# Kernel optimization log

Hardware: AMD Instinct MI355X
Metric: run time of the kernel (lower is better)

The kernel has to match this reference:

```python
import jax, jax.numpy as jnp
import numpy as np
import math

D_MODEL = 512
N_HEADS = 8
WINDOW = 5
B, S = 4, 2048


def setup_inputs() -> dict:
    key = jax.random.key(0)
    ks = jax.random.split(key, 16)
    d = D_MODEL

    def lin(k, fan_in, fan_out):
        bound = 1.0 / math.sqrt(fan_in)
        kw, kb = jax.random.split(k)
        W = jax.random.uniform(kw, (fan_in, fan_out), jnp.float32, -bound, bound)
        b = jax.random.uniform(kb, (fan_out,), jnp.float32, -bound, bound)
        return W, b

    x = jax.random.normal(ks[0], (B, S, d), jnp.float32)
    W1, b1 = lin(ks[1], d, 2 * d)      # mapping layer 1
    W2, b2 = lin(ks[2], 2 * d, d)      # mapping layer 2
    Wq, bq = lin(ks[3], d, d)
    Wk, bk = lin(ks[4], d, d)
    Wv, bv = lin(ks[5], d, d)
    Wo, bo = lin(ks[6], d, d)
    return dict(x=x, W1=W1, b1=b1, W2=W2, b2=b2, Wq=Wq, bq=bq,
                Wk=Wk, bk=bk, Wv=Wv, bv=bv, Wo=Wo, bo=bo)


def reference(x, W1, b1, W2, b2, Wq, bq, Wk, bk, Wv, bv, Wo, bo):
    Bsz, S_, d = x.shape
    h = N_HEADS
    hd = d // h

    # mapping MLP: Linear -> ReLU -> Linear
    xm = jax.nn.relu(x @ W1 + b1) @ W2 + b2

    def split_heads(t):  # [B,S,d] -> [B,h,S,hd]
        return t.reshape(Bsz, S_, h, hd).transpose(0, 2, 1, 3)

    Q = split_heads(xm @ Wq + bq)
    K = split_heads(xm @ Wk + bk)
    V = split_heads(xm @ Wv + bv)

    scores = jnp.einsum('bhqd,bhkd->bhqk', Q, K) / math.sqrt(hd)

    # inverse sliding-window mask: positions with |i-j| <= window are EXCLUDED
    idx = jnp.arange(S_)
    adjacent = jnp.abs(idx[:, None] - idx[None, :]) <= WINDOW  # [S,S] bool
    scores = jnp.where(adjacent[None, None], -1e9, scores)

    attn = jax.nn.softmax(scores, axis=-1)
    out = jnp.einsum('bhqk,bhkd->bhqd', attn, V)
    out = out.transpose(0, 2, 1, 3).reshape(Bsz, S_, d)
    return out @ Wo + bo
```

## Files before the change

### kernel.cpp

```cpp
#include <hip/hip_runtime.h>
#include <stdint.h>

typedef __attribute__((ext_vector_type(8))) short bf16x8;
typedef __attribute__((ext_vector_type(4))) float f32x4;

__device__ __forceinline__ float bf2f(uint16_t u) {
    union { uint32_t u; float f; } c; c.u = ((uint32_t)u) << 16; return c.f;
}
__device__ __forceinline__ uint16_t f2bf(float f) {
    union { float f; uint32_t u; } c; c.f = f;
    uint32_t r = c.u + 0x7fffu + ((c.u >> 16) & 1u);
    return (uint16_t)(r >> 16);
}
__device__ __forceinline__ uint32_t pk2bf(float a, float b) {
#if __has_builtin(__builtin_amdgcn_cvt_pk_bf16_f32)
    auto v = __builtin_amdgcn_cvt_pk_bf16_f32(a, b);
    uint32_t u; __builtin_memcpy(&u, &v, 4); return u;
#else
    return (uint32_t)f2bf(a) | ((uint32_t)f2bf(b) << 16);
#endif
}
__device__ __forceinline__ float fexp2(float x) {
#if __has_builtin(__builtin_amdgcn_exp2f)
    return __builtin_amdgcn_exp2f(x);
#else
    return exp2f(x);
#endif
}

__device__ __forceinline__ void gld_lds16(const uint16_t* g, uint16_t* l) {
    __builtin_amdgcn_global_load_lds(
        (const __attribute__((address_space(1))) void*)g,
        (__attribute__((address_space(3))) void*)l, 16, 0, 0);
}

__global__ void prep_all(const float* __restrict__ x,
                         const float* __restrict__ W1, const float* __restrict__ W2,
                         const float* __restrict__ Wq, const float* __restrict__ Wk,
                         const float* __restrict__ Wv, const float* __restrict__ Wo,
                         const float* __restrict__ b1, const float* __restrict__ b2,
                         const float* __restrict__ bq, const float* __restrict__ bk,
                         const float* __restrict__ bv, const float* __restrict__ bo,
                         uint16_t* __restrict__ W1T, uint16_t* __restrict__ W2T,
                         uint16_t* __restrict__ WqkvT, uint16_t* __restrict__ WoT,
                         uint16_t* __restrict__ xb, uint16_t* __restrict__ bbase)
{
    const int id = blockIdx.x;
    const int tx = threadIdx.x, ty = threadIdx.y;
    const int tid = ty * 32 + tx;
    if (id < 2048) {
        __shared__ uint16_t t[32][33];
        const float* src; uint16_t* dst; int R, C, tile;
        if      (id < 512)  { src = W1; dst = W1T;              R = 512;  C = 1024; tile = id; }
        else if (id < 1024) { src = W2; dst = W2T;              R = 1024; C = 512;  tile = id - 512; }
        else if (id < 1280) { src = Wq; dst = WqkvT;            R = 512;  C = 512;  tile = id - 1024; }
        else if (id < 1536) { src = Wk; dst = WqkvT + 512*512;  R = 512;  C = 512;  tile = id - 1280; }
        else if (id < 1792) { src = Wv; dst = WqkvT + 1024*512; R = 512;  C = 512;  tile = id - 1536; }
        else                { src = Wo; dst = WoT;              R = 512;  C = 512;  tile = id - 1792; }
        const int ntx = C / 32;
        const int bx = (tile % ntx) * 32, by = (tile / ntx) * 32;
#pragma unroll
        for (int i = ty; i < 32; i += 8) t[i][tx] = f2bf(src[(size_t)(by + i) * C + bx + tx]);
        __syncthreads();
#pragma unroll
        for (int i = ty; i < 32; i += 8) dst[(size_t)(bx + i) * R + by + tx] = t[tx][i];
    } else if (id < 6144) {
        int i = (id - 2048) * 256 + tid;
        float4 v = ((const float4*)x)[i];
        ushort4 o;
        o.x = f2bf(v.x); o.y = f2bf(v.y); o.z = f2bf(v.z); o.w = f2bf(v.w);
        ((ushort4*)xb)[i] = o;
    } else {
        int i = (id - 6144) * 256 + tid;
        if      (i < 1024) bbase[i] = f2bf(b1[i]);
        else if (i < 1536) bbase[i] = f2bf(b2[i - 1024]);
        else if (i < 2048) bbase[i] = f2bf(bq[i - 1536]);
        else if (i < 2560) bbase[i] = f2bf(bk[i - 2048]);
        else if (i < 3072) bbase[i] = f2bf(bv[i - 2560]);
        else if (i < 3584) bbase[i] = f2bf(bo[i - 3072]);
    }
}

template<int RELU, int F32OUT>
__global__ __launch_bounds__(256, 3)
void gemm_k64(const uint16_t* __restrict__ A, const uint16_t* __restrict__ Bt,
              const uint16_t* __restrict__ bias, void* __restrict__ Cv,
              int M, int N, int K)
{
    __shared__ __align__(16) uint16_t lsA[2][64 * 64];
    __shared__ __align__(16) uint16_t lsB[2][128 * 64];

    const int tid = threadIdx.x, lane = tid & 63;
    const int wid = tid >> 6;
    const int quad = lane >> 4, lm = lane & 15;
    const int wm = wid >> 1, wn = wid & 1;
    const int m0 = blockIdx.y * 64, n0 = blockIdx.x * 128;

    f32x4 acc[2][4];
#pragma unroll
    for (int i = 0; i < 2; ++i)
#pragma unroll
        for (int j = 0; j < 4; ++j) acc[i][j] = (f32x4){0.f, 0.f, 0.f, 0.f};

    auto stage = [&](int k0, int bb) {
#pragma unroll
        for (int c4 = 0; c4 < 2; ++c4) {
            const int chunk = c4 * 256 + tid;
            const int r = chunk >> 3, lc = (chunk & 7) ^ (r & 7);
            gld_lds16(A + (size_t)(m0 + r) * K + k0 + lc * 8, &lsA[bb][(size_t)chunk * 8]);
        }
#pragma unroll
        for (int c4 = 0; c4 < 4; ++c4) {
            const int chunk = c4 * 256 + tid;
            const int r = chunk >> 3, lc = (chunk & 7) ^ (r & 7);
            gld_lds16(Bt + (size_t)(n0 + r) * K + k0 + lc * 8, &lsB[bb][(size_t)chunk * 8]);
        }
    };
    auto compute = [&](int bb) {
#pragma unroll
        for (int kh = 0; kh < 2; ++kh) {
            const int pc = ((kh * 4 + quad) ^ (lm & 7));
            bf16x8 af[2], bfr[4];
#pragma unroll
            for (int t = 0; t < 2; ++t)
                af[t] = *(const bf16x8*)(&lsA[bb][(wm * 32 + t * 16 + lm) * 64 + pc * 8]);
#pragma unroll
            for (int t = 0; t < 4; ++t)
                bfr[t] = *(const bf16x8*)(&lsB[bb][(wn * 64 + t * 16 + lm) * 64 + pc * 8]);
#pragma unroll
            for (int i = 0; i < 2; ++i)
#pragma unroll
                for (int j = 0; j < 4; ++j)
                    acc[i][j] = __builtin_amdgcn_mfma_f32_16x16x32_bf16(af[i], bfr[j], acc[i][j], 0, 0, 0);
        }
    };

    stage(0, 0);
    int cur = 0;
#pragma unroll 1
    for (int k0 = 64; k0 < K; k0 += 64) {
        stage(k0, cur ^ 1);
        asm volatile("s_waitcnt vmcnt(6)" ::: "memory");
        __builtin_amdgcn_sched_barrier(0);
        __builtin_amdgcn_s_barrier();
        compute(cur);
        __builtin_amdgcn_s_barrier();
        cur ^= 1;
    }
    asm volatile("s_waitcnt vmcnt(0)" ::: "memory");
    __builtin_amdgcn_sched_barrier(0);
    __builtin_amdgcn_s_barrier();
    compute(cur);

#pragma unroll
    for (int i = 0; i < 2; ++i) {
        const int r0 = m0 + wm * 32 + i * 16 + quad * 4;
#pragma unroll
        for (int j = 0; j < 4; ++j) {
            const int col = n0 + wn * 64 + j * 16 + lm;
            const float bvj = bf2f(bias[col]);
#pragma unroll
            for (int r = 0; r < 4; ++r) {
                float v = acc[i][j][r] + bvj;
                if (RELU) v = fmaxf(v, 0.f);
                if (F32OUT) ((float*)Cv)[(size_t)(r0 + r) * N + col] = v;
                else        ((uint16_t*)Cv)[(size_t)(r0 + r) * N + col] = f2bf(v);
            }
        }
    }
}

template<int RELU, int F32OUT>
__global__ __launch_bounds__(256, 4)
void gemm_k32(const uint16_t* __restrict__ A, const uint16_t* __restrict__ Bt,
              const uint16_t* __restrict__ bias, void* __restrict__ Cv,
              int M, int N, int K)
{
    __shared__ __align__(16) uint16_t lsA[2][32 * 64];
    __shared__ __align__(16) uint16_t lsB[2][128 * 64];

    const int tid = threadIdx.x, lane = tid & 63;
    const int wid = tid >> 6;
    const int quad = lane >> 4, lm = lane & 15;
    const int wm = wid >> 1, wn = wid & 1;
    const int m0 = blockIdx.y * 32, n0 = blockIdx.x * 128;

    f32x4 acc[4];
#pragma unroll
    for (int j = 0; j < 4; ++j) acc[j] = (f32x4){0.f, 0.f, 0.f, 0.f};

    auto stage = [&](int k0, int bb) {
        {
            const int chunk = tid;
            const int r = chunk >> 3, lc = (chunk & 7) ^ (r & 7);
            gld_lds16(A + (size_t)(m0 + r) * K + k0 + lc * 8, &lsA[bb][(size_t)chunk * 8]);
        }
#pragma unroll
        for (int c4 = 0; c4 < 4; ++c4) {
            const int chunk = c4 * 256 + tid;
            const int r = chunk >> 3, lc = (chunk & 7) ^ (r & 7);
            gld_lds16(Bt + (size_t)(n0 + r) * K + k0 + lc * 8, &lsB[bb][(size_t)chunk * 8]);
        }
    };
    auto compute = [&](int bb) {
#pragma unroll
        for (int kh = 0; kh < 2; ++kh) {
            const int pc = ((kh * 4 + quad) ^ (lm & 7));
            bf16x8 af = *(const bf16x8*)(&lsA[bb][(wm * 16 + lm) * 64 + pc * 8]);
            bf16x8 bfr[4];
#pragma unroll
            for (int t = 0; t < 4; ++t)
                bfr[t] = *(const bf16x8*)(&lsB[bb][(wn * 64 + t * 16 + lm) * 64 + pc * 8]);
#pragma unroll
            for (int j = 0; j < 4; ++j)
                acc[j] = __builtin_amdgcn_mfma_f32_16x16x32_bf16(af, bfr[j], acc[j], 0, 0, 0);
        }
    };

    stage(0, 0);
    int cur = 0;
#pragma unroll 1
    for (int k0 = 64; k0 < K; k0 += 64) {
        stage(k0, cur ^ 1);
        asm volatile("s_waitcnt vmcnt(5)" ::: "memory");
        __builtin_amdgcn_sched_barrier(0);
        __builtin_amdgcn_s_barrier();
        compute(cur);
        __builtin_amdgcn_s_barrier();
        cur ^= 1;
    }
    asm volatile("s_waitcnt vmcnt(0)" ::: "memory");
    __builtin_amdgcn_sched_barrier(0);
    __builtin_amdgcn_s_barrier();
    compute(cur);

    const int r0 = m0 + wm * 16 + quad * 4;
#pragma unroll
    for (int j = 0; j < 4; ++j) {
        const int col = n0 + wn * 64 + j * 16 + lm;
        const float bvj = bf2f(bias[col]);
#pragma unroll
        for (int r = 0; r < 4; ++r) {
            float v = acc[j][r] + bvj;
            if (RELU) v = fmaxf(v, 0.f);
            if (F32OUT) ((float*)Cv)[(size_t)(r0 + r) * N + col] = v;
            else        ((uint16_t*)Cv)[(size_t)(r0 + r) * N + col] = f2bf(v);
        }
    }
}

__global__ __launch_bounds__(256, 3)
void gemm_qkv64(const uint16_t* __restrict__ A, const uint16_t* __restrict__ Bt,
                const uint16_t* __restrict__ bq, const uint16_t* __restrict__ bk,
                const uint16_t* __restrict__ bv_,
                uint16_t* __restrict__ qk, uint16_t* __restrict__ Vt)
{
    __shared__ __align__(16) uint16_t lsA[2][64 * 64];
    __shared__ __align__(16) uint16_t lsB[2][128 * 64];

    const int tid = threadIdx.x, lane = tid & 63;
    const int wid = tid >> 6;
    const int quad = lane >> 4, lm = lane & 15;
    const int wm = wid >> 1, wn = wid & 1;
    const int m0 = blockIdx.y * 64, n0 = blockIdx.x * 128;
    const int part = n0 >> 9;
    const uint16_t* B = (part == 0) ? bq : (part == 1) ? bk : bv_;
    const int K = 512;

    f32x4 acc[2][4];
#pragma unroll
    for (int i = 0; i < 2; ++i)
#pragma unroll
        for (int j = 0; j < 4; ++j) acc[i][j] = (f32x4){0.f, 0.f, 0.f, 0.f};

    auto stage = [&](int k0, int bb) {
#pragma unroll
        for (int c4 = 0; c4 < 2; ++c4) {
            const int chunk = c4 * 256 + tid;
            const int r = chunk >> 3, lc = (chunk & 7) ^ (r & 7);
            gld_lds16(A + (size_t)(m0 + r) * K + k0 + lc * 8, &lsA[bb][(size_t)chunk * 8]);
        }
#pragma unroll
        for (int c4 = 0; c4 < 4; ++c4) {
            const int chunk = c4 * 256 + tid;
            const int r = chunk >> 3, lc = (chunk & 7) ^ (r & 7);
            gld_lds16(Bt + (size_t)(n0 + r) * K + k0 + lc * 8, &lsB[bb][(size_t)chunk * 8]);
        }
    };
    auto compute = [&](int bb) {
#pragma unroll
        for (int kh = 0; kh < 2; ++kh) {
            const int pc = ((kh * 4 + quad) ^ (lm & 7));
            bf16x8 af[2], bfr[4];
#pragma unroll
            for (int t = 0; t < 2; ++t)
                af[t] = *(const bf16x8*)(&lsA[bb][(wm * 32 + t * 16 + lm) * 64 + pc * 8]);
#pragma unroll
            for (int t = 0; t < 4; ++t)
                bfr[t] = *(const bf16x8*)(&lsB[bb][(wn * 64 + t * 16 + lm) * 64 + pc * 8]);
#pragma unroll
            for (int i = 0; i < 2; ++i)
#pragma unroll
                for (int j = 0; j < 4; ++j)
                    acc[i][j] = __builtin_amdgcn_mfma_f32_16x16x32_bf16(af[i], bfr[j], acc[i][j], 0, 0, 0);
        }
    };

    stage(0, 0);
    int cur = 0;
#pragma unroll 1
    for (int k0 = 64; k0 < K; k0 += 64) {
        stage(k0, cur ^ 1);
        asm volatile("s_waitcnt vmcnt(6)" ::: "memory");
        __builtin_amdgcn_sched_barrier(0);
        __builtin_amdgcn_s_barrier();
        compute(cur);
        __builtin_amdgcn_s_barrier();
        cur ^= 1;
    }
    asm volatile("s_waitcnt vmcnt(0)" ::: "memory");
    __builtin_amdgcn_sched_barrier(0);
    __builtin_amdgcn_s_barrier();
    compute(cur);

#pragma unroll
    for (int i = 0; i < 2; ++i) {
        const int mb = m0 + wm * 32 + i * 16 + quad * 4;
#pragma unroll
        for (int j = 0; j < 4; ++j) {
            const int nl = (n0 & 511) + wn * 64 + j * 16 + lm;
            const float bvj = bf2f(B[nl]);
            if (part < 2) {
#pragma unroll
                for (int r = 0; r < 4; ++r)
                    qk[(size_t)(mb + r) * 1024 + part * 512 + nl] = f2bf(acc[i][j][r] + bvj);
            } else {
                const int h = nl >> 6, d = nl & 63;
                const int b = mb >> 11, s0 = mb & 2047;
                const int sp = (s0 & ~31) | ((s0 & 12) << 1) | (((s0 >> 4) & 1) << 2);
                const size_t base = ((size_t)(((b << 3) | h)) * 64 + d) * 2048 + sp;
#pragma unroll
                for (int r = 0; r < 4; ++r)
                    Vt[base + r] = f2bf(acc[i][j][r] + bvj);
            }
        }
    }
}

__global__ __launch_bounds__(512, 4)
void attn_k(const uint16_t* __restrict__ qk, const uint16_t* __restrict__ Vt,
            uint16_t* __restrict__ Out)
{
    __shared__ __align__(16) uint16_t lsAll[2][16384];

    const int tid = threadIdx.x, lane = tid & 63, wid = tid >> 6;
    const int qw = wid & 3, kh2 = wid >> 2;
    const int quad = lane >> 4, lm = lane & 15;
    const int bh = blockIdx.y, b = bh >> 3, h = bh & 7;
    const int q0 = blockIdx.x * 128;
    const float cscale = 0.125f * 1.44269504088896f;

    bf16x8 qf[2][2];
#pragma unroll
    for (int i = 0; i < 2; ++i)
#pragma unroll
        for (int ks = 0; ks < 2; ++ks) {
            bf16x8 q = *(const bf16x8*)(qk +
                (size_t)(b * 2048 + q0 + qw * 32 + i * 16 + lm) * 1024 + h * 64 + ks * 32 + quad * 8);
#pragma unroll
            for (int e = 0; e < 8; ++e)
                q[e] = (short)f2bf(bf2f((uint16_t)q[e]) * cscale);
            qf[i][ks] = q;
        }

    f32x4 oacc[2][4];
#pragma unroll
    for (int i = 0; i < 2; ++i)
#pragma unroll
        for (int n = 0; n < 4; ++n) oacc[i][n] = (f32x4){0.f, 0.f, 0.f, 0.f};
    float lrow[2] = {0.f, 0.f};

    auto stage = [&](int j0, int bb) {
        uint16_t* lsK = &lsAll[bb][0];
        uint16_t* lsV = &lsAll[bb][8192];
#pragma unroll
        for (int c2 = 0; c2 < 2; ++c2) {
            const int chunk = c2 * 512 + tid;
            const int r = chunk >> 3, lc = (chunk & 7) ^ (r & 7);
            gld_lds16(qk + (size_t)(b * 2048 + j0 + r) * 1024 + 512 + h * 64 + lc * 8,
                      lsK + (size_t)chunk * 8);
        }
#pragma unroll
        for (int c2 = 0; c2 < 2; ++c2) {
            const int chunk = c2 * 512 + tid;
            const int d = chunk >> 4, lc = (chunk & 15) ^ (d & 15);
            gld_lds16(Vt + (size_t)(bh * 64 + d) * 2048 + j0 + lc * 8,
                      lsV + (size_t)chunk * 8);
        }
    };

    auto compute = [&](int j0, int bb) {
        const uint16_t* Kb = &lsAll[bb][0];
        const uint16_t* Vb = &lsAll[bb][8192];

        f32x4 sacc[2][4];
#pragma unroll
        for (int i = 0; i < 2; ++i)
#pragma unroll
            for (int j = 0; j < 4; ++j) sacc[i][j] = (f32x4){0.f, 0.f, 0.f, 0.f};
        __builtin_amdgcn_s_setprio(1);
#pragma unroll
        for (int ks = 0; ks < 2; ++ks)
#pragma unroll
            for (int j = 0; j < 4; ++j) {
                const int pc = (ks * 4 + quad) ^ (lm & 7);
                bf16x8 kf = *(const bf16x8*)(Kb + (kh2 * 64 + j * 16 + lm) * 64 + pc * 8);
#pragma unroll
                for (int i = 0; i < 2; ++i)
                    sacc[i][j] = __builtin_amdgcn_mfma_f32_16x16x32_bf16(kf, qf[i][ks], sacc[i][j], 0, 0, 0);
            }
        __builtin_amdgcn_s_setprio(0);

        if ((j0 + 127 >= q0 - 5) && (j0 <= q0 + 127 + 5)) {
#pragma unroll
            for (int i = 0; i < 2; ++i) {
                const int qr = q0 + qw * 32 + i * 16 + lm;
#pragma unroll
                for (int j = 0; j < 4; ++j)
#pragma unroll
                    for (int r = 0; r < 4; ++r) {
                        int kc = j0 + kh2 * 64 + j * 16 + quad * 4 + r;
                        int dd = qr - kc; if (dd < 0) dd = -dd;
                        if (dd <= 5) sacc[i][j][r] = -1e30f;
                    }
            }
        }

#pragma unroll
        for (int ksl = 0; ksl < 2; ++ksl) {
            const int gs = kh2 * 2 + ksl;
            bf16x8 pa[2];
#pragma unroll
            for (int i = 0; i < 2; ++i) {
                const float p0 = fexp2(sacc[i][2 * ksl + 0][0]);
                const float p1 = fexp2(sacc[i][2 * ksl + 0][1]);
                const float p2 = fexp2(sacc[i][2 * ksl + 0][2]);
                const float p3 = fexp2(sacc[i][2 * ksl + 0][3]);
                const float p4 = fexp2(sacc[i][2 * ksl + 1][0]);
                const float p5 = fexp2(sacc[i][2 * ksl + 1][1]);
                const float p6 = fexp2(sacc[i][2 * ksl + 1][2]);
                const float p7 = fexp2(sacc[i][2 * ksl + 1][3]);
                lrow[i] += ((p0 + p1) + (p2 + p3)) + ((p4 + p5) + (p6 + p7));
                union { bf16x8 v; uint32_t u[4]; } c;
                c.u[0] = pk2bf(p0, p1);
                c.u[1] = pk2bf(p2, p3);
                c.u[2] = pk2bf(p4, p5);
                c.u[3] = pk2bf(p6, p7);
                pa[i] = c.v;
            }
            __builtin_amdgcn_s_setprio(1);
#pragma unroll
            for (int n = 0; n < 4; ++n) {
                const int pc = (gs * 4 + quad) ^ lm;
                bf16x8 vf = *(const bf16x8*)(Vb + (n * 16 + lm) * 128 + pc * 8);
#pragma unroll
                for (int i = 0; i < 2; ++i)
                    oacc[i][n] = __builtin_amdgcn_mfma_f32_16x16x32_bf16(pa[i], vf, oacc[i][n], 0, 0, 0);
            }
            __builtin_amdgcn_s_setprio(0);
        }
    };

    stage(0, 0);
    int cur = 0;
#pragma unroll 1
    for (int jt = 0; jt < 15; ++jt) {
        stage((jt + 1) * 128, cur ^ 1);
        asm volatile("s_waitcnt vmcnt(4)" ::: "memory");
        __builtin_amdgcn_sched_barrier(0);
        __builtin_amdgcn_s_barrier();
        compute(jt * 128, cur);
        __builtin_amdgcn_s_barrier();
        cur ^= 1;
    }
    asm volatile("s_waitcnt vmcnt(0)" ::: "memory");
    __builtin_amdgcn_sched_barrier(0);
    __builtin_amdgcn_s_barrier();
    compute(15 * 128, cur);

    __syncthreads();
    f32x4* red = (f32x4*)&lsAll[0][0];
    if (wid >= 4) {
        const int base = ((wid - 4) * 64 + lane) * 9;
#pragma unroll
        for (int i = 0; i < 2; ++i)
#pragma unroll
            for (int n = 0; n < 4; ++n) red[base + i * 4 + n] = oacc[i][n];
        red[base + 8] = (f32x4){lrow[0], lrow[1], 0.f, 0.f};
    }
    __syncthreads();
    if (wid < 4) {
        const int base = (wid * 64 + lane) * 9;
#pragma unroll
        for (int i = 0; i < 2; ++i)
#pragma unroll
            for (int n = 0; n < 4; ++n) oacc[i][n] += red[base + i * 4 + n];
        const f32x4 lr = red[base + 8];
        lrow[0] += lr[0]; lrow[1] += lr[1];

#pragma unroll
        for (int i = 0; i < 2; ++i) {
            float l = lrow[i];
            l += __shfl_xor(l, 16);
            l += __shfl_xor(l, 32);
            const float inv = 1.f / (l + 1e-30f);
#pragma unroll
            for (int r = 0; r < 4; ++r) {
                const float invr = __shfl(inv, quad * 4 + r, 16);
                const int s = q0 + wid * 32 + i * 16 + quad * 4 + r;
#pragma unroll
                for (int n = 0; n < 4; ++n)
                    Out[(size_t)(b * 2048 + s) * 512 + h * 64 + n * 16 + lm] = f2bf(oacc[i][n][r] * invr);
            }
        }
    }
}

extern "C" void kernel_launch(void* const* d_in, const int* in_sizes, int n_in,
                              void* d_out, int out_size, void* d_ws, size_t ws_size,
                              hipStream_t stream)
{
    const float* x  = (const float*)d_in[0];
    const float* W1 = (const float*)d_in[1];
    const float* b1 = (const float*)d_in[2];
    const float* W2 = (const float*)d_in[3];
    const float* b2 = (const float*)d_in[4];
    const float* Wq = (const float*)d_in[5];
    const float* bq = (const float*)d_in[6];
    const float* Wk = (const float*)d_in[7];
    const float* bk = (const float*)d_in[8];
    const float* Wv = (const float*)d_in[9];
    const float* bv = (const float*)d_in[10];
    const float* Wo = (const float*)d_in[11];
    const float* bo = (const float*)d_in[12];
    (void)in_sizes; (void)n_in; (void)out_size; (void)ws_size;

    char* ws = (char*)d_ws;
    const size_t MiB = 1024 * 1024;
    uint16_t* xb    = (uint16_t*)(ws + 0);
    uint16_t* W1T   = (uint16_t*)(ws + 8 * MiB);
    uint16_t* W2T   = (uint16_t*)(ws + 9 * MiB);
    uint16_t* WqkvT = (uint16_t*)(ws + 10 * MiB);
    uint16_t* WoT   = (uint16_t*)(ws + 11 * MiB + 512 * 1024);
    uint16_t* bbase = (uint16_t*)(ws + 12 * MiB);
    uint16_t* b1b = bbase, *b2b = bbase + 1024, *bqb = bbase + 1536;
    uint16_t* bkb = bbase + 2048, *bvb = bbase + 2560, *bob = bbase + 3072;
    uint16_t* xm1   = (uint16_t*)(ws + 13 * MiB);
    uint16_t* xm    = (uint16_t*)(ws + 29 * MiB);
    uint16_t* qk    = xm1;
    uint16_t* att   = xm;
    uint16_t* Vt    = xb;

    prep_all<<<6158, dim3(32, 8), 0, stream>>>(x, W1, W2, Wq, Wk, Wv, Wo,
                                               b1, b2, bq, bk, bv, bo,
                                               W1T, W2T, WqkvT, WoT, xb, bbase);

    gemm_k64<1,0><<<dim3(8, 128),  256, 0, stream>>>(xb,  W1T, b1b, xm1, 8192, 1024, 512);
    gemm_k32<0,0><<<dim3(4, 256),  256, 0, stream>>>(xm1, W2T, b2b, xm,  8192, 512, 1024);
    gemm_qkv64   <<<dim3(12, 128), 256, 0, stream>>>(xm, WqkvT, bqb, bkb, bvb, qk, Vt);
    attn_k       <<<dim3(16, 32),  512, 0, stream>>>(qk, Vt, att);
    gemm_k32<0,1><<<dim3(4, 256),  256, 0, stream>>>(att, WoT, bob, d_out, 8192, 512, 512);
}
```

Measured before the change: 211.6 us.

## Enlarge first MLP GEMM tile, stage V transpose through LDS, remap attention blocks

The first mapping GEMM becomes a specialised 256x128-tile kernel with 512 threads and a 4x4 MFMA accumulator per wave, which raises operand reuse per LDS load. The V output of the QKV GEMM is now transposed through shared memory and written to Vt as 16-byte vector stores instead of scattered 2-byte stores. The attention grid is remapped so that consecutive block IDs round-robin across the 8 XCDs while each XCD keeps the same batch-heads, aiming for better L2 locality of K/V. The larger GEMM tile uses more LDS and registers per block and produces fewer blocks (256), which lowers occupancy.

After: 216.0 us. 1.02x slower.

```diff
diff --git a/kernel.cpp b/kernel.cpp
--- a/kernel.cpp
+++ b/kernel.cpp
@@ -81,37 +81,36 @@
     }
 }
 
-template<int RELU, int F32OUT>
-__global__ __launch_bounds__(256, 3)
-void gemm_k64(const uint16_t* __restrict__ A, const uint16_t* __restrict__ Bt,
-              const uint16_t* __restrict__ bias, void* __restrict__ Cv,
-              int M, int N, int K)
+__global__ __launch_bounds__(512, 2)
+void gemm_g1_256(const uint16_t* __restrict__ A, const uint16_t* __restrict__ Bt,
+                 const uint16_t* __restrict__ bias, uint16_t* __restrict__ C)
 {
-    __shared__ __align__(16) uint16_t lsA[2][64 * 64];
+    __shared__ __align__(16) uint16_t lsA[2][256 * 64];
     __shared__ __align__(16) uint16_t lsB[2][128 * 64];
 
     const int tid = threadIdx.x, lane = tid & 63;
     const int wid = tid >> 6;
     const int quad = lane >> 4, lm = lane & 15;
     const int wm = wid >> 1, wn = wid & 1;
-    const int m0 = blockIdx.y * 64, n0 = blockIdx.x * 128;
-
-    f32x4 acc[2][4];
-#pragma unroll
-    for (int i = 0; i < 2; ++i)
+    const int m0 = blockIdx.y * 256, n0 = blockIdx.x * 128;
+    const int K = 512, N = 1024;
+
+    f32x4 acc[4][4];
+#pragma unroll
+    for (int i = 0; i < 4; ++i)
 #pragma unroll
         for (int j = 0; j < 4; ++j) acc[i][j] = (f32x4){0.f, 0.f, 0.f, 0.f};
 
     auto stage = [&](int k0, int bb) {
 #pragma unroll
-        for (int c4 = 0; c4 < 2; ++c4) {
-            const int chunk = c4 * 256 + tid;
+        for (int c4 = 0; c4 < 4; ++c4) {
+            const int chunk = c4 * 512 + tid;
             const int r = chunk >> 3, lc = (chunk & 7) ^ (r & 7);
             gld_lds16(A + (size_t)(m0 + r) * K + k0 + lc * 8, &lsA[bb][(size_t)chunk * 8]);
         }
 #pragma unroll
-        for (int c4 = 0; c4 < 4; ++c4) {
-            const int chunk = c4 * 256 + tid;
+        for (int c2 = 0; c2 < 2; ++c2) {
+            const int chunk = c2 * 512 + tid;
             const int r = chunk >> 3, lc = (chunk & 7) ^ (r & 7);
             gld_lds16(Bt + (size_t)(n0 + r) * K + k0 + lc * 8, &lsB[bb][(size_t)chunk * 8]);
         }
@@ -120,15 +119,14 @@
 #pragma unroll
         for (int kh = 0; kh < 2; ++kh) {
             const int pc = ((kh * 4 + quad) ^ (lm & 7));
-            bf16x8 af[2], bfr[4];
-#pragma unroll
-            for (int t = 0; t < 2; ++t)
-                af[t] = *(const bf16x8*)(&lsA[bb][(wm * 32 + t * 16 + lm) * 64 + pc * 8]);
-#pragma unroll
-            for (int t = 0; t < 4; ++t)
+            bf16x8 af[4], bfr[4];
+#pragma unroll
+            for (int t = 0; t < 4; ++t) {
+                af[t]  = *(const bf16x8*)(&lsA[bb][(wm * 64 + t * 16 + lm) * 64 + pc * 8]);
                 bfr[t] = *(const bf16x8*)(&lsB[bb][(wn * 64 + t * 16 + lm) * 64 + pc * 8]);
-#pragma unroll
-            for (int i = 0; i < 2; ++i)
+            }
+#pragma unroll
+            for (int i = 0; i < 4; ++i)
 #pragma unroll
                 for (int j = 0; j < 4; ++j)
                     acc[i][j] = __builtin_amdgcn_mfma_f32_16x16x32_bf16(af[i], bfr[j], acc[i][j], 0, 0, 0);
@@ -153,18 +151,16 @@
     compute(cur);
 
 #pragma unroll
-    for (int i = 0; i < 2; ++i) {
-        const int r0 = m0 + wm * 32 + i * 16 + quad * 4;
+    for (int i = 0; i < 4; ++i) {
+        const int r0 = m0 + wm * 64 + i * 16 + quad * 4;
 #pragma unroll
         for (int j = 0; j < 4; ++j) {
             const int col = n0 + wn * 64 + j * 16 + lm;
             const float bvj = bf2f(bias[col]);
 #pragma unroll
             for (int r = 0; r < 4; ++r) {
-                float v = acc[i][j][r] + bvj;
-                if (RELU) v = fmaxf(v, 0.f);
-                if (F32OUT) ((float*)Cv)[(size_t)(r0 + r) * N + col] = v;
-                else        ((uint16_t*)Cv)[(size_t)(r0 + r) * N + col] = f2bf(v);
+                float v = fmaxf(acc[i][j][r] + bvj, 0.f);
+                C[(size_t)(r0 + r) * N + col] = f2bf(v);
             }
         }
     }
@@ -323,26 +319,45 @@
     __builtin_amdgcn_s_barrier();
     compute(cur);
 
-#pragma unroll
-    for (int i = 0; i < 2; ++i) {
-        const int mb = m0 + wm * 32 + i * 16 + quad * 4;
-#pragma unroll
-        for (int j = 0; j < 4; ++j) {
-            const int nl = (n0 & 511) + wn * 64 + j * 16 + lm;
-            const float bvj = bf2f(B[nl]);
-            if (part < 2) {
+    if (part < 2) {
+#pragma unroll
+        for (int i = 0; i < 2; ++i) {
+            const int mb = m0 + wm * 32 + i * 16 + quad * 4;
+#pragma unroll
+            for (int j = 0; j < 4; ++j) {
+                const int nl = (n0 & 511) + wn * 64 + j * 16 + lm;
+                const float bvj = bf2f(B[nl]);
 #pragma unroll
                 for (int r = 0; r < 4; ++r)
                     qk[(size_t)(mb + r) * 1024 + part * 512 + nl] = f2bf(acc[i][j][r] + bvj);
-            } else {
-                const int h = nl >> 6, d = nl & 63;
-                const int b = mb >> 11, s0 = mb & 2047;
-                const int sp = (s0 & ~31) | ((s0 & 12) << 1) | (((s0 >> 4) & 1) << 2);
-                const size_t base = ((size_t)(((b << 3) | h)) * 64 + d) * 2048 + sp;
-#pragma unroll
-                for (int r = 0; r < 4; ++r)
-                    Vt[base + r] = f2bf(acc[i][j][r] + bvj);
-            }
+            }
+        }
+    } else {
+        __syncthreads();
+        uint16_t* tb = &lsB[0][0];
+#pragma unroll
+        for (int i = 0; i < 2; ++i) {
+#pragma unroll
+            for (int j = 0; j < 4; ++j) {
+                const int hd = wn * 64 + j * 16 + lm;
+                const float bvj = bf2f(B[(n0 & 511) + hd]);
+#pragma unroll
+                for (int r = 0; r < 4; ++r) {
+                    const int kk = wm * 32 + i * 16 + quad * 4 + r;
+                    const int kp = (kk & 32) | ((kk & 12) << 1) | (((kk >> 4) & 1) << 2) | (kk & 3);
+                    tb[hd * 64 + (kp ^ ((hd & 7) << 3))] = f2bf(acc[i][j][r] + bvj);
+                }
+            }
+        }
+        __syncthreads();
+        const int b = m0 >> 11, s0 = m0 & 2047, h0 = (n0 & 511) >> 6;
+#pragma unroll
+        for (int t2 = 0; t2 < 4; ++t2) {
+            const int task = t2 * 256 + tid;
+            const int hd = task >> 3, seg = task & 7;
+            const bf16x8 v = *(const bf16x8*)(tb + hd * 64 + ((seg ^ (hd & 7)) << 3));
+            const int hh = h0 + (hd >> 6), d = hd & 63;
+            *(bf16x8*)(Vt + ((size_t)((b << 3) | hh) * 64 + d) * 2048 + s0 + seg * 8) = v;
         }
     }
 }
@@ -356,8 +371,10 @@
     const int tid = threadIdx.x, lane = tid & 63, wid = tid >> 6;
     const int qw = wid & 3, kh2 = wid >> 2;
     const int quad = lane >> 4, lm = lane & 15;
-    const int bh = blockIdx.y, b = bh >> 3, h = bh & 7;
-    const int q0 = blockIdx.x * 128;
+    const int ib = blockIdx.y * 16 + blockIdx.x;
+    const int xcd = ib & 7, kq = ib >> 3;
+    const int bh = xcd * 4 + (kq >> 4), q0 = (kq & 15) * 128;
+    const int b = bh >> 3, h = bh & 7;
     const float cscale = 0.125f * 1.44269504088896f;
 
     bf16x8 qf[2][2];
@@ -565,8 +582,8 @@
                                                b1, b2, bq, bk, bv, bo,
                                                W1T, W2T, WqkvT, WoT, xb, bbase);
 
-    gemm_k64<1,0><<<dim3(8, 128),  256, 0, stream>>>(xb,  W1T, b1b, xm1, 8192, 1024, 512);
-    gemm_k32<0,0><<<dim3(4, 256),  256, 0, stream>>>(xm1, W2T, b2b, xm,  8192, 512, 1024);
+    gemm_g1_256  <<<dim3(8, 32),   512, 0, stream>>>(xb, W1T, b1b, xm1);
+    gemm_k32<0,0><<<dim3(4, 256),  256, 0, stream>>>(xm1, W2T, b2b, xm, 8192, 512, 1024);
     gemm_qkv64   <<<dim3(12, 128), 256, 0, stream>>>(xm, WqkvT, bqb, bkb, bvb, qk, Vt);
     attn_k       <<<dim3(16, 32),  512, 0, stream>>>(qk, Vt, att);
     gemm_k32<0,1><<<dim3(4, 256),  256, 0, stream>>>(att, WoT, bob, d_out, 8192, 512, 512);
```
